# Optimization experiments

Hardware: AMD Instinct MI355X
Metric: run time of the kernel (lower is better)

## Reference

```python
import jax, jax.numpy as jnp
import numpy as np

B, NQ, NK = 4, 384, 384
D_EQUI, D_QINV, D_KVINV = 64, 256, 256
D_MSG, D_FF, D_OUT = 64, 128, 64
IN_FEATS = 2 * D_MSG + D_EQUI  # 192


def setup_inputs() -> dict:
    key = jax.random.key(0)
    ks = jax.random.split(key, 12)
    s = lambda k, shp, fan: jax.random.normal(k, shp, jnp.float32) / np.sqrt(fan)
    return {
        "q_equi": jax.random.normal(ks[0], (B, NQ, 3, D_EQUI), jnp.float32),
        "q_inv": jax.random.normal(ks[1], (B, NQ, D_QINV), jnp.float32),
        "k_equi": jax.random.normal(ks[2], (B, NK, 3, D_EQUI), jnp.float32),
        "k_inv": jax.random.normal(ks[3], (B, NK, D_KVINV), jnp.float32),
        "Wq": s(ks[4], (D_QINV, D_MSG), D_QINV),
        "bq": jnp.zeros((D_MSG,), jnp.float32),
        "Wk": s(ks[5], (D_KVINV, D_MSG), D_KVINV),
        "bk": jnp.zeros((D_MSG,), jnp.float32),
        "W1": s(ks[6], (IN_FEATS, D_FF), IN_FEATS),
        "b1": jnp.zeros((D_FF,), jnp.float32),
        "W2": s(ks[7], (D_FF, D_OUT), D_FF),
        "b2": jnp.zeros((D_OUT,), jnp.float32),
    }


def reference(q_equi, q_inv, k_equi, k_inv, Wq, bq, Wk, bk, W1, b1, W2, b2):
    # dotprods over the 3 spatial coords, per equi-channel: [B, Nq, Nk, d_equi]
    dotprods = jnp.einsum("bqcd,bkcd->bqkd", q_equi, k_equi)
    q_msg = q_inv @ Wq + bq  # [B, Nq, d_msg]
    k_msg = k_inv @ Wk + bk  # [B, Nk, d_msg]
    b, nq, dm = q_msg.shape
    nk = k_msg.shape[1]
    # expand + concat -> [B, Nq, Nk, in_feats]
    feats = jnp.concatenate(
        [
            jnp.broadcast_to(q_msg[:, :, None, :], (b, nq, nk, dm)),
            jnp.broadcast_to(k_msg[:, None, :, :], (b, nq, nk, dm)),
            dotprods,
        ],
        axis=-1,
    )
    h = jax.nn.silu(feats @ W1 + b1)  # [B, Nq, Nk, d_ff]
    return h @ W2 + b2  # [B, Nq, Nk, d_out]
```

## Files before the change

kernel.cpp:

```cpp
#include <hip/hip_runtime.h>
#include <hip/hip_bf16.h>
#include <stdint.h>
#include <stddef.h>

#define NQ 384
#define NK 384

typedef __attribute__((ext_vector_type(4))) float float4_;
typedef __attribute__((ext_vector_type(8))) short short8;
typedef __attribute__((ext_vector_type(2))) unsigned int uint2_;

__device__ __forceinline__ short f2bf(float f) {
  union { float f; uint32_t u; } v; v.f = f;
  uint32_t u = v.u;
  uint32_t r = (u + 0x7fffu + ((u >> 16) & 1u)) >> 16;
  return (short)r;
}

__device__ __forceinline__ unsigned int pk2(float lo, float hi) {
  __hip_bfloat162 r = __float22bfloat162_rn(make_float2(lo, hi));
  union { __hip_bfloat162 b; unsigned int u; } u; u.b = r;
  return u.u;
}

__global__ __launch_bounds__(256) void prep0(
    const float* __restrict__ Wq, const float* __restrict__ Wk,
    const float* __restrict__ W1, const float* __restrict__ b1,
    const float* __restrict__ bq, const float* __restrict__ bk,
    const float* __restrict__ W2,
    float* __restrict__ Wqc, float* __restrict__ Wkc,
    float* __restrict__ c1, float* __restrict__ c2,
    short* __restrict__ W1dfrag, short* __restrict__ W2frag)
{
  int bid = blockIdx.x, t = threadIdx.x;
  if (bid < 32) {
    int side = bid >> 4;
    int r0 = (bid & 15) * 16;
    const float* W = side ? Wk : Wq;
    const float* W1s = W1 + side * 64 * 128;
    float* Wc = side ? Wkc : Wqc;
    __shared__ float sW[16][64];
    for (int j = t; j < 1024; j += 256) sW[j >> 6][j & 63] = W[(r0 + (j >> 6)) * 64 + (j & 63)];
    __syncthreads();
    int c = t & 127, rg = (t >> 7) * 8;
    float acc[8] = {0.f, 0.f, 0.f, 0.f, 0.f, 0.f, 0.f, 0.f};
    for (int k = 0; k < 64; ++k) {
      float wv = W1s[k * 128 + c];
      #pragma unroll
      for (int j = 0; j < 8; ++j) acc[j] += sW[rg + j][k] * wv;
    }
    for (int j = 0; j < 8; ++j) Wc[(r0 + rg + j) * 128 + c] = acc[j];
  } else if (bid == 32) {
    if (t < 256) {
      int c = t & 127, side = t >> 7;
      const float* bias = side ? bk : bq;
      const float* W1s = W1 + side * 64 * 128;
      float acc = side ? 0.f : b1[c];
      for (int k = 0; k < 64; ++k) acc += bias[k] * W1s[k * 128 + c];
      (side ? c2 : c1)[c] = acc;
    }
  } else {
    for (int idx = t; idx < 8192; idx += 256) {
      int fi = idx >> 9;
      int l  = (idx >> 3) & 63;
      int i  = idx & 7;
      { int n = fi >> 1, s = fi & 1;
        int d = s * 32 + ((l >> 4) << 3) + i;
        int f = n * 16 + (l & 15);
        W1dfrag[idx] = f2bf(W1[(128 + d) * 128 + f]); }
      { int n2 = fi >> 2, s2 = fi & 3;
        int k = s2 * 32 + ((l >> 4) << 3) + i;
        int o = n2 * 16 + (l & 15);
        W2frag[idx] = f2bf(W2[k * 64 + o]); }
    }
  }
}

__global__ __launch_bounds__(256) void prep1(
    const float* __restrict__ q_inv, const float* __restrict__ k_inv,
    const float* __restrict__ Wqc, const float* __restrict__ Wkc,
    const float* __restrict__ c1, const float* __restrict__ c2,
    float* __restrict__ A1, float* __restrict__ A2)
{
  int bid = blockIdx.x, t = threadIdx.x;
  int row0 = bid * 8;
  int side = row0 >= 1536;
  int r0 = row0 - side * 1536;
  const float* inv = (side ? k_inv : q_inv) + (size_t)r0 * 256;
  const float* Wc  = side ? Wkc : Wqc;
  const float* cc  = side ? c2 : c1;
  float* A = (side ? A2 : A1) + (size_t)r0 * 128;

  __shared__ float sI[8][256];
  for (int j = t; j < 2048; j += 256) sI[j >> 8][j & 255] = inv[j];
  __syncthreads();

  int c = t & 127, rg = (t >> 7) * 4;
  float acc[4] = {0.f, 0.f, 0.f, 0.f};
  for (int k = 0; k < 256; ++k) {
    float wv = Wc[k * 128 + c];
    #pragma unroll
    for (int j = 0; j < 4; ++j) acc[j] += sI[rg + j][k] * wv;
  }
  float cv = cc[c];
  #pragma unroll
  for (int j = 0; j < 4; ++j) A[(size_t)(rg + j) * 128 + c] = acc[j] + cv;
}

__global__ __launch_bounds__(512) void main_kernel(
    const float* __restrict__ q_equi, const float* __restrict__ k_equi,
    const float* __restrict__ A1, const float* __restrict__ A2,
    const short* __restrict__ W1dfrag, const short* __restrict__ W2frag,
    const float* __restrict__ b2, float* __restrict__ out)
{
  int bid = blockIdx.x;
  int b = bid / 576;
  int rem = bid - b * 576;
  int tq = rem / 24, tk = rem - (rem / 24) * 24;
  int q0 = tq * 16, k0 = tk * 16;

  __shared__ __align__(16) char smem[32768];
  float* sQ = (float*)smem;
  float* sK = (float*)(smem + 13056);

  int tid = threadIdx.x;
  int w = tid >> 6, l = tid & 63;
  int g = l >> 4, r16 = l & 15;

  const float* qsrc = q_equi + ((size_t)(b * NQ + q0)) * 192;
  const float* ksrc = k_equi + ((size_t)(b * NK + k0)) * 192;
  for (int j = tid; j < 3072; j += 512) {
    int rr = j / 192, cd = j - rr * 192;
    int c = cd >> 6, d = cd & 63;
    int li = c * 1088 + rr * 68 + d;
    sQ[li] = qsrc[j];
    sK[li] = ksrc[j];
  }
  __syncthreads();

  short8 afrag[2][2];
  #pragma unroll
  for (int s = 0; s < 2; ++s) {
    int d0 = s * 32 + g * 8;
    float4_ kva[3], kvb[3];
    #pragma unroll
    for (int c = 0; c < 3; ++c) {
      kva[c] = *(const float4_*)&sK[c * 1088 + r16 * 68 + d0];
      kvb[c] = *(const float4_*)&sK[c * 1088 + r16 * 68 + d0 + 4];
    }
    #pragma unroll
    for (int m = 0; m < 2; ++m) {
      int qi = 2 * w + m;
      float4_ qva[3], qvb[3];
      #pragma unroll
      for (int c = 0; c < 3; ++c) {
        qva[c] = *(const float4_*)&sQ[c * 1088 + qi * 68 + d0];
        qvb[c] = *(const float4_*)&sQ[c * 1088 + qi * 68 + d0 + 4];
      }
      float da[4], db[4];
      #pragma unroll
      for (int i = 0; i < 4; ++i) {
        da[i] = qva[0][i] * kva[0][i] + qva[1][i] * kva[1][i] + qva[2][i] * kva[2][i];
        db[i] = qvb[0][i] * kvb[0][i] + qvb[1][i] * kvb[1][i] + qvb[2][i] * kvb[2][i];
      }
      union { short8 s8; unsigned int u[4]; } au;
      au.u[0] = pk2(da[0], da[1]);
      au.u[1] = pk2(da[2], da[3]);
      au.u[2] = pk2(db[0], db[1]);
      au.u[3] = pk2(db[2], db[3]);
      afrag[m][s] = au.s8;
    }
  }
  __syncthreads();

  char* hbase = smem + w * 4096;
  const float* A1p = A1 + ((size_t)(b * NQ + q0)) * 128;
  const float* A2p = A2 + ((size_t)(b * NK + k0)) * 128;

  float4_ b2v[4];
  #pragma unroll
  for (int ot = 0; ot < 4; ++ot)
    b2v[ot] = *(const float4_*)&b2[ot * 16 + g * 4];

  #pragma unroll
  for (int m = 0; m < 2; ++m) {
    int qi = 2 * w + m;

    float4_ acc1[8];
    #pragma unroll
    for (int ft = 0; ft < 8; ++ft) {
      float4_ a1v = *(const float4_*)&A1p[qi * 128 + ft * 16 + g * 4];
      float4_ a2v = *(const float4_*)&A2p[r16 * 128 + ft * 16 + g * 4];
      acc1[ft] = a1v + a2v;
    }

    #pragma unroll
    for (int ft = 0; ft < 8; ++ft) {
      #pragma unroll
      for (int s = 0; s < 2; ++s) {
        short8 wf = *(const short8*)&W1dfrag[(((ft * 2 + s) * 64) + l) * 8];
        acc1[ft] = __builtin_amdgcn_mfma_f32_16x16x32_bf16(wf, afrag[m][s], acc1[ft], 0, 0, 0);
      }
    }

    #pragma unroll
    for (int ft = 0; ft < 8; ++ft) {
      float4_ x = acc1[ft];
      float y0 = x[0] / (1.f + __expf(-x[0]));
      float y1 = x[1] / (1.f + __expf(-x[1]));
      float y2 = x[2] / (1.f + __expf(-x[2]));
      float y3 = x[3] / (1.f + __expf(-x[3]));
      uint2_ pv;
      pv[0] = pk2(y0, y1);
      pv[1] = pk2(y2, y3);
      int byte = (r16 * 256 + ft * 32 + g * 8) ^ ((r16 & 7) << 4);
      *(uint2_*)(hbase + byte) = pv;
    }

    float4_ acc2[4];
    #pragma unroll
    for (int ot = 0; ot < 4; ++ot) acc2[ot] = (float4_){0.f, 0.f, 0.f, 0.f};
    #pragma unroll
    for (int s2 = 0; s2 < 4; ++s2) {
      int byte = (r16 * 256 + s2 * 64 + g * 16) ^ ((r16 & 7) << 4);
      short8 hb = *(const short8*)(hbase + byte);
      #pragma unroll
      for (int ot = 0; ot < 4; ++ot) {
        short8 wf = *(const short8*)&W2frag[(((ot * 4 + s2) * 64) + l) * 8];
        acc2[ot] = __builtin_amdgcn_mfma_f32_16x16x32_bf16(wf, hb, acc2[ot], 0, 0, 0);
      }
    }

    float* op = out + ((size_t)(b * NQ + q0 + qi) * NK + k0 + r16) * 64;
    #pragma unroll
    for (int ot = 0; ot < 4; ++ot) {
      float4_ o4 = acc2[ot] + b2v[ot];
      *(float4_*)(op + ot * 16 + g * 4) = o4;
    }
  }
}

extern "C" void kernel_launch(void* const* d_in, const int* in_sizes, int n_in,
                              void* d_out, int out_size, void* d_ws, size_t ws_size,
                              hipStream_t stream) {
  (void)in_sizes; (void)n_in; (void)out_size; (void)ws_size;
  const float* q_equi = (const float*)d_in[0];
  const float* q_inv  = (const float*)d_in[1];
  const float* k_equi = (const float*)d_in[2];
  const float* k_inv  = (const float*)d_in[3];
  const float* Wq = (const float*)d_in[4];
  const float* bq = (const float*)d_in[5];
  const float* Wk = (const float*)d_in[6];
  const float* bk = (const float*)d_in[7];
  const float* W1 = (const float*)d_in[8];
  const float* b1 = (const float*)d_in[9];
  const float* W2 = (const float*)d_in[10];
  const float* b2 = (const float*)d_in[11];
  float* out = (float*)d_out;

  char* ws = (char*)d_ws;
  float* A1      = (float*)(ws);
  float* A2      = (float*)(ws + 786432);
  short* W1dfrag = (short*)(ws + 1572864);
  short* W2frag  = (short*)(ws + 1589248);
  float* Wqc     = (float*)(ws + 1605632);
  float* Wkc     = (float*)(ws + 1736704);
  float* c1      = (float*)(ws + 1867776);
  float* c2      = (float*)(ws + 1868288);

  prep0<<<34, 256, 0, stream>>>(Wq, Wk, W1, b1, bq, bk, W2, Wqc, Wkc, c1, c2, W1dfrag, W2frag);
  prep1<<<384, 256, 0, stream>>>(q_inv, k_inv, Wqc, Wkc, c1, c2, A1, A2);
  main_kernel<<<2304, 512, 0, stream>>>(q_equi, k_equi, A1, A2, W1dfrag, W2frag, b2, out);
}
```

Before: 295.3 us.

## Double q-tile per block, keep W1 fragments in registers, stage W2 in LDS

Each block now covers 32 q rows instead of 16 and loops four q rows per wave, which halves the grid. The W1 MFMA fragments are loaded once into registers and reused across rows, and W2 fragments are staged once in shared memory rather than reread from global per row. q_equi is now read straight from global per row instead of through LDS, and the b2 bias is folded into the accumulator init. The larger LDS footprint, the register-resident W1 fragments and launch_bounds(512,2) may limit occupancy or cause spills.

```diff
diff --git a/kernel.cpp b/kernel.cpp
--- a/kernel.cpp
+++ b/kernel.cpp
@@ -107,84 +107,90 @@
   for (int j = 0; j < 4; ++j) A[(size_t)(rg + j) * 128 + c] = acc[j] + cv;
 }
 
-__global__ __launch_bounds__(512) void main_kernel(
+__global__ __launch_bounds__(512, 2) void main_kernel(
     const float* __restrict__ q_equi, const float* __restrict__ k_equi,
     const float* __restrict__ A1, const float* __restrict__ A2,
     const short* __restrict__ W1dfrag, const short* __restrict__ W2frag,
     const float* __restrict__ b2, float* __restrict__ out)
 {
   int bid = blockIdx.x;
-  int b = bid / 576;
-  int rem = bid - b * 576;
+  int b = bid / 288;
+  int rem = bid - b * 288;
   int tq = rem / 24, tk = rem - (rem / 24) * 24;
-  int q0 = tq * 16, k0 = tk * 16;
-
-  __shared__ __align__(16) char smem[32768];
-  float* sQ = (float*)smem;
-  float* sK = (float*)(smem + 13056);
+  int q0 = tq * 32, k0 = tk * 16;
+
+  __shared__ __align__(16) char smem[62208];
+  float* sK  = (float*)smem;
+  short* sW2 = (short*)(smem + 13056);
+  char*  hall = smem + 29440;
 
   int tid = threadIdx.x;
   int w = tid >> 6, l = tid & 63;
   int g = l >> 4, r16 = l & 15;
 
-  const float* qsrc = q_equi + ((size_t)(b * NQ + q0)) * 192;
   const float* ksrc = k_equi + ((size_t)(b * NK + k0)) * 192;
-  for (int j = tid; j < 3072; j += 512) {
+  #pragma unroll
+  for (int it = 0; it < 6; ++it) {
+    int j = tid + it * 512;
     int rr = j / 192, cd = j - rr * 192;
     int c = cd >> 6, d = cd & 63;
-    int li = c * 1088 + rr * 68 + d;
-    sQ[li] = qsrc[j];
-    sK[li] = ksrc[j];
-  }
+    sK[c * 1088 + rr * 68 + d] = ksrc[j];
+  }
+  {
+    short8 v0 = *(const short8*)&W2frag[tid * 8];
+    short8 v1 = *(const short8*)&W2frag[(tid + 512) * 8];
+    *(short8*)&sW2[tid * 8] = v0;
+    *(short8*)&sW2[(tid + 512) * 8] = v1;
+  }
+  short8 w1f[8][2];
+  #pragma unroll
+  for (int ft = 0; ft < 8; ++ft)
+    #pragma unroll
+    for (int s = 0; s < 2; ++s)
+      w1f[ft][s] = *(const short8*)&W1dfrag[(((ft * 2 + s) * 64) + l) * 8];
+
+  float4_ b2v[4];
+  #pragma unroll
+  for (int ot = 0; ot < 4; ++ot)
+    b2v[ot] = *(const float4_*)&b2[ot * 16 + g * 4];
+
   __syncthreads();
 
-  short8 afrag[2][2];
-  #pragma unroll
-  for (int s = 0; s < 2; ++s) {
-    int d0 = s * 32 + g * 8;
-    float4_ kva[3], kvb[3];
-    #pragma unroll
-    for (int c = 0; c < 3; ++c) {
-      kva[c] = *(const float4_*)&sK[c * 1088 + r16 * 68 + d0];
-      kvb[c] = *(const float4_*)&sK[c * 1088 + r16 * 68 + d0 + 4];
-    }
-    #pragma unroll
-    for (int m = 0; m < 2; ++m) {
-      int qi = 2 * w + m;
-      float4_ qva[3], qvb[3];
+  char* hbase = hall + w * 4096;
+  const float* A1p = A1 + ((size_t)(b * NQ + q0)) * 128;
+  const float* A2p = A2 + ((size_t)(b * NK + k0)) * 128;
+  const float* qrow_base = q_equi + ((size_t)(b * NQ + q0)) * 192;
+
+  #pragma unroll 1
+  for (int qq = 0; qq < 4; ++qq) {
+    int qi = w * 4 + qq;
+    const float* qrow = qrow_base + (size_t)qi * 192;
+
+    short8 afrag[2];
+    #pragma unroll
+    for (int s = 0; s < 2; ++s) {
+      int d0 = s * 32 + g * 8;
+      float da[4] = {0.f, 0.f, 0.f, 0.f};
+      float db[4] = {0.f, 0.f, 0.f, 0.f};
       #pragma unroll
       for (int c = 0; c < 3; ++c) {
-        qva[c] = *(const float4_*)&sQ[c * 1088 + qi * 68 + d0];
-        qvb[c] = *(const float4_*)&sQ[c * 1088 + qi * 68 + d0 + 4];
-      }
-      float da[4], db[4];
-      #pragma unroll
-      for (int i = 0; i < 4; ++i) {
-        da[i] = qva[0][i] * kva[0][i] + qva[1][i] * kva[1][i] + qva[2][i] * kva[2][i];
-        db[i] = qvb[0][i] * kvb[0][i] + qvb[1][i] * kvb[1][i] + qvb[2][i] * kvb[2][i];
+        float4_ kva = *(const float4_*)&sK[c * 1088 + r16 * 68 + d0];
+        float4_ kvb = *(const float4_*)&sK[c * 1088 + r16 * 68 + d0 + 4];
+        float4_ qva = *(const float4_*)&qrow[c * 64 + d0];
+        float4_ qvb = *(const float4_*)&qrow[c * 64 + d0 + 4];
+        #pragma unroll
+        for (int i = 0; i < 4; ++i) {
+          da[i] += qva[i] * kva[i];
+          db[i] += qvb[i] * kvb[i];
+        }
       }
       union { short8 s8; unsigned int u[4]; } au;
       au.u[0] = pk2(da[0], da[1]);
       au.u[1] = pk2(da[2], da[3]);
       au.u[2] = pk2(db[0], db[1]);
       au.u[3] = pk2(db[2], db[3]);
-      afrag[m][s] = au.s8;
-    }
-  }
-  __syncthreads();
-
-  char* hbase = smem + w * 4096;
-  const float* A1p = A1 + ((size_t)(b * NQ + q0)) * 128;
-  const float* A2p = A2 + ((size_t)(b * NK + k0)) * 128;
-
-  float4_ b2v[4];
-  #pragma unroll
-  for (int ot = 0; ot < 4; ++ot)
-    b2v[ot] = *(const float4_*)&b2[ot * 16 + g * 4];
-
-  #pragma unroll
-  for (int m = 0; m < 2; ++m) {
-    int qi = 2 * w + m;
+      afrag[s] = au.s8;
+    }
 
     float4_ acc1[8];
     #pragma unroll
@@ -193,15 +199,11 @@
       float4_ a2v = *(const float4_*)&A2p[r16 * 128 + ft * 16 + g * 4];
       acc1[ft] = a1v + a2v;
     }
-
-    #pragma unroll
-    for (int ft = 0; ft < 8; ++ft) {
-      #pragma unroll
-      for (int s = 0; s < 2; ++s) {
-        short8 wf = *(const short8*)&W1dfrag[(((ft * 2 + s) * 64) + l) * 8];
-        acc1[ft] = __builtin_amdgcn_mfma_f32_16x16x32_bf16(wf, afrag[m][s], acc1[ft], 0, 0, 0);
-      }
-    }
+    #pragma unroll
+    for (int ft = 0; ft < 8; ++ft)
+      #pragma unroll
+      for (int s = 0; s < 2; ++s)
+        acc1[ft] = __builtin_amdgcn_mfma_f32_16x16x32_bf16(w1f[ft][s], afrag[s], acc1[ft], 0, 0, 0);
 
     #pragma unroll
     for (int ft = 0; ft < 8; ++ft) {
@@ -219,24 +221,22 @@
 
     float4_ acc2[4];
     #pragma unroll
-    for (int ot = 0; ot < 4; ++ot) acc2[ot] = (float4_){0.f, 0.f, 0.f, 0.f};
+    for (int ot = 0; ot < 4; ++ot) acc2[ot] = b2v[ot];
     #pragma unroll
     for (int s2 = 0; s2 < 4; ++s2) {
       int byte = (r16 * 256 + s2 * 64 + g * 16) ^ ((r16 & 7) << 4);
       short8 hb = *(const short8*)(hbase + byte);
       #pragma unroll
       for (int ot = 0; ot < 4; ++ot) {
-        short8 wf = *(const short8*)&W2frag[(((ot * 4 + s2) * 64) + l) * 8];
+        short8 wf = *(const short8*)&sW2[(((ot * 4 + s2) * 64) + l) * 8];
         acc2[ot] = __builtin_amdgcn_mfma_f32_16x16x32_bf16(wf, hb, acc2[ot], 0, 0, 0);
       }
     }
 
     float* op = out + ((size_t)(b * NQ + q0 + qi) * NK + k0 + r16) * 64;
     #pragma unroll
-    for (int ot = 0; ot < 4; ++ot) {
-      float4_ o4 = acc2[ot] + b2v[ot];
-      *(float4_*)(op + ot * 16 + g * 4) = o4;
-    }
+    for (int ot = 0; ot < 4; ++ot)
+      *(float4_*)(op + ot * 16 + g * 4) = acc2[ot];
   }
 }
 
@@ -270,5 +270,5 @@
 
   prep0<<<34, 256, 0, stream>>>(Wq, Wk, W1, b1, bq, bk, W2, Wqc, Wkc, c1, c2, W1dfrag, W2frag);
   prep1<<<384, 256, 0, stream>>>(q_inv, k_inv, Wqc, Wkc, c1, c2, A1, A2);
-  main_kernel<<<2304, 512, 0, stream>>>(q_equi, k_equi, A1, A2, W1dfrag, W2frag, b2, out);
-}
+  main_kernel<<<1152, 512, 0, stream>>>(q_equi, k_equi, A1, A2, W1dfrag, W2frag, b2, out);
+}
```

Measured after the change: 319.1 us. +8.1%, slower.

## Interleave MFMA over two query rows, drop Q smem staging, remap block order

Applied to the files above, without the earlier changes.

Restructures the main kernel so each wave runs both of its query rows through the two MFMA stages together, loading each W1/W2 fragment once and issuing two independent MFMAs per fragment. Q equivariant data is now read straight from global memory instead of being staged in shared memory, leaving only K in LDS. The bias b2 is folded into the accumulator's initial value. Block indices are remapped with an 8-way interleave, which changes which tiles run next to each other and is likely aimed at cache locality or spreading blocks across dies. The cost is more live registers (two accumulator sets plus held H fragments), which may reduce occupancy.

```diff
diff --git a/kernel.cpp b/kernel.cpp
--- a/kernel.cpp
+++ b/kernel.cpp
@@ -113,31 +113,31 @@
     const short* __restrict__ W1dfrag, const short* __restrict__ W2frag,
     const float* __restrict__ b2, float* __restrict__ out)
 {
-  int bid = blockIdx.x;
+  int bid0 = blockIdx.x;
+  int bid = (bid0 & 7) * 288 + (bid0 >> 3);
   int b = bid / 576;
   int rem = bid - b * 576;
   int tq = rem / 24, tk = rem - (rem / 24) * 24;
   int q0 = tq * 16, k0 = tk * 16;
 
   __shared__ __align__(16) char smem[32768];
-  float* sQ = (float*)smem;
-  float* sK = (float*)(smem + 13056);
+  float* sK = (float*)smem;
 
   int tid = threadIdx.x;
   int w = tid >> 6, l = tid & 63;
   int g = l >> 4, r16 = l & 15;
 
-  const float* qsrc = q_equi + ((size_t)(b * NQ + q0)) * 192;
   const float* ksrc = k_equi + ((size_t)(b * NK + k0)) * 192;
-  for (int j = tid; j < 3072; j += 512) {
+  #pragma unroll
+  for (int it = 0; it < 6; ++it) {
+    int j = tid + it * 512;
     int rr = j / 192, cd = j - rr * 192;
     int c = cd >> 6, d = cd & 63;
-    int li = c * 1088 + rr * 68 + d;
-    sQ[li] = qsrc[j];
-    sK[li] = ksrc[j];
+    sK[c * 1088 + rr * 68 + d] = ksrc[j];
   }
   __syncthreads();
 
+  const float* qrow0 = q_equi + ((size_t)(b * NQ + q0 + 2 * w)) * 192;
   short8 afrag[2][2];
   #pragma unroll
   for (int s = 0; s < 2; ++s) {
@@ -150,18 +150,18 @@
     }
     #pragma unroll
     for (int m = 0; m < 2; ++m) {
-      int qi = 2 * w + m;
-      float4_ qva[3], qvb[3];
+      const float* qrow = qrow0 + m * 192;
+      float da[4] = {0.f, 0.f, 0.f, 0.f};
+      float db[4] = {0.f, 0.f, 0.f, 0.f};
       #pragma unroll
       for (int c = 0; c < 3; ++c) {
-        qva[c] = *(const float4_*)&sQ[c * 1088 + qi * 68 + d0];
-        qvb[c] = *(const float4_*)&sQ[c * 1088 + qi * 68 + d0 + 4];
-      }
-      float da[4], db[4];
-      #pragma unroll
-      for (int i = 0; i < 4; ++i) {
-        da[i] = qva[0][i] * kva[0][i] + qva[1][i] * kva[1][i] + qva[2][i] * kva[2][i];
-        db[i] = qvb[0][i] * kvb[0][i] + qvb[1][i] * kvb[1][i] + qvb[2][i] * kvb[2][i];
+        float4_ qva = *(const float4_*)&qrow[c * 64 + d0];
+        float4_ qvb = *(const float4_*)&qrow[c * 64 + d0 + 4];
+        #pragma unroll
+        for (int i = 0; i < 4; ++i) {
+          da[i] += qva[i] * kva[c][i];
+          db[i] += qvb[i] * kvb[c][i];
+        }
       }
       union { short8 s8; unsigned int u[4]; } au;
       au.u[0] = pk2(da[0], da[1]);
@@ -173,39 +173,34 @@
   }
   __syncthreads();
 
+  const float* A1p = A1 + ((size_t)(b * NQ + q0 + 2 * w)) * 128;
+  const float* A2p = A2 + ((size_t)(b * NK + k0)) * 128;
+  float4_ acc1[2][8];
+  #pragma unroll
+  for (int ft = 0; ft < 8; ++ft) {
+    float4_ a2v = *(const float4_*)&A2p[r16 * 128 + ft * 16 + g * 4];
+    acc1[0][ft] = *(const float4_*)&A1p[ft * 16 + g * 4] + a2v;
+    acc1[1][ft] = *(const float4_*)&A1p[128 + ft * 16 + g * 4] + a2v;
+  }
+
+  #pragma unroll
+  for (int ft = 0; ft < 8; ++ft) {
+    #pragma unroll
+    for (int s = 0; s < 2; ++s) {
+      short8 wf = *(const short8*)&W1dfrag[(((ft * 2 + s) * 64) + l) * 8];
+      #pragma unroll
+      for (int m = 0; m < 2; ++m)
+        acc1[m][ft] = __builtin_amdgcn_mfma_f32_16x16x32_bf16(wf, afrag[m][s], acc1[m][ft], 0, 0, 0);
+    }
+  }
+
   char* hbase = smem + w * 4096;
-  const float* A1p = A1 + ((size_t)(b * NQ + q0)) * 128;
-  const float* A2p = A2 + ((size_t)(b * NK + k0)) * 128;
-
-  float4_ b2v[4];
-  #pragma unroll
-  for (int ot = 0; ot < 4; ++ot)
-    b2v[ot] = *(const float4_*)&b2[ot * 16 + g * 4];
-
+  short8 hb[2][4];
   #pragma unroll
   for (int m = 0; m < 2; ++m) {
-    int qi = 2 * w + m;
-
-    float4_ acc1[8];
     #pragma unroll
     for (int ft = 0; ft < 8; ++ft) {
-      float4_ a1v = *(const float4_*)&A1p[qi * 128 + ft * 16 + g * 4];
-      float4_ a2v = *(const float4_*)&A2p[r16 * 128 + ft * 16 + g * 4];
-      acc1[ft] = a1v + a2v;
-    }
-
-    #pragma unroll
-    for (int ft = 0; ft < 8; ++ft) {
-      #pragma unroll
-      for (int s = 0; s < 2; ++s) {
-        short8 wf = *(const short8*)&W1dfrag[(((ft * 2 + s) * 64) + l) * 8];
-        acc1[ft] = __builtin_amdgcn_mfma_f32_16x16x32_bf16(wf, afrag[m][s], acc1[ft], 0, 0, 0);
-      }
-    }
-
-    #pragma unroll
-    for (int ft = 0; ft < 8; ++ft) {
-      float4_ x = acc1[ft];
+      float4_ x = acc1[m][ft];
       float y0 = x[0] / (1.f + __expf(-x[0]));
       float y1 = x[1] / (1.f + __expf(-x[1]));
       float y2 = x[2] / (1.f + __expf(-x[2]));
@@ -216,27 +211,39 @@
       int byte = (r16 * 256 + ft * 32 + g * 8) ^ ((r16 & 7) << 4);
       *(uint2_*)(hbase + byte) = pv;
     }
-
-    float4_ acc2[4];
-    #pragma unroll
-    for (int ot = 0; ot < 4; ++ot) acc2[ot] = (float4_){0.f, 0.f, 0.f, 0.f};
     #pragma unroll
     for (int s2 = 0; s2 < 4; ++s2) {
       int byte = (r16 * 256 + s2 * 64 + g * 16) ^ ((r16 & 7) << 4);
-      short8 hb = *(const short8*)(hbase + byte);
-      #pragma unroll
-      for (int ot = 0; ot < 4; ++ot) {
-        short8 wf = *(const short8*)&W2frag[(((ot * 4 + s2) * 64) + l) * 8];
-        acc2[ot] = __builtin_amdgcn_mfma_f32_16x16x32_bf16(wf, hb, acc2[ot], 0, 0, 0);
-      }
-    }
-
-    float* op = out + ((size_t)(b * NQ + q0 + qi) * NK + k0 + r16) * 64;
+      hb[m][s2] = *(const short8*)(hbase + byte);
+    }
+  }
+
+  float4_ b2v[4];
+  #pragma unroll
+  for (int ot = 0; ot < 4; ++ot)
+    b2v[ot] = *(const float4_*)&b2[ot * 16 + g * 4];
+  float4_ acc2[2][4];
+  #pragma unroll
+  for (int m = 0; m < 2; ++m)
+    #pragma unroll
+    for (int ot = 0; ot < 4; ++ot) acc2[m][ot] = b2v[ot];
+  #pragma unroll
+  for (int s2 = 0; s2 < 4; ++s2) {
     #pragma unroll
     for (int ot = 0; ot < 4; ++ot) {
-      float4_ o4 = acc2[ot] + b2v[ot];
-      *(float4_*)(op + ot * 16 + g * 4) = o4;
-    }
+      short8 wf = *(const short8*)&W2frag[(((ot * 4 + s2) * 64) + l) * 8];
+      #pragma unroll
+      for (int m = 0; m < 2; ++m)
+        acc2[m][ot] = __builtin_amdgcn_mfma_f32_16x16x32_bf16(wf, hb[m][s2], acc2[m][ot], 0, 0, 0);
+    }
+  }
+
+  #pragma unroll
+  for (int m = 0; m < 2; ++m) {
+    float* op = out + ((size_t)(b * NQ + q0 + 2 * w + m) * NK + k0 + r16) * 64;
+    #pragma unroll
+    for (int ot = 0; ot < 4; ++ot)
+      *(float4_*)(op + ot * 16 + g * 4) = acc2[m][ot];
   }
 }
 
```

After: 261.5 us. -11.4%, faster.
